# Optimization experiments

Measured on AMD Instinct MI355X. Metric: run time of the kernel, lower is better.

Reference implementation:

```python
import jax, jax.numpy as jnp
import numpy as np

B, C, CI, T, H, W = 4, 256, 128, 8, 28, 28
EPS = 1e-5


def setup_inputs() -> dict:
    key = jax.random.key(0)
    ks = jax.random.split(key, 12)
    s = 0.02
    return {
        "x": jax.random.normal(ks[0], (B, C, T, H, W), jnp.float32),
        "Wg": jax.random.normal(ks[1], (CI, C), jnp.float32) * s,
        "bg": jax.random.normal(ks[2], (CI,), jnp.float32) * s,
        "Wt": jax.random.normal(ks[3], (CI, C), jnp.float32) * s,
        "bt": jax.random.normal(ks[4], (CI,), jnp.float32) * s,
        "Wp": jax.random.normal(ks[5], (CI, C), jnp.float32) * s,
        "bp": jax.random.normal(ks[6], (CI,), jnp.float32) * s,
        "Ww": jax.random.normal(ks[7], (C, CI), jnp.float32) * s,
        "bw": jax.random.normal(ks[8], (C,), jnp.float32) * s,
        "gamma": jax.random.normal(ks[9], (C,), jnp.float32) * s + 1.0,
        "beta": jax.random.normal(ks[10], (C,), jnp.float32) * s,
        "rmean": jax.random.normal(ks[11], (C,), jnp.float32) * s,
        "rvar": jax.random.uniform(jax.random.fold_in(key, 99), (C,), jnp.float32, 0.5, 1.5),
    }


def reference(x, Wg, bg, Wt, bt, Wp, bp, Ww, bw, gamma, beta, rmean, rvar):
    b, c, t, h, w = x.shape
    n = t * h * w
    xf = x.reshape(b, c, n)                                   # [B,C,N]
    # 1x1x1 conv projections == per-position linear maps
    g = jnp.einsum('oc,bcn->bno', Wg, xf) + bg                # [B,N,Ci]
    th = jnp.einsum('oc,bcn->bno', Wt, xf) + bt               # [B,N,Ci]
    ph = jnp.einsum('oc,bcn->bon', Wp, xf) + bp[None, :, None]  # [B,Ci,N]
    f = jnp.einsum('bnc,bcm->bnm', th, ph)                    # [B,N,N] attention logits
    attn = jax.nn.softmax(f, axis=-1)
    y = jnp.einsum('bnm,bmo->bno', attn, g)                   # [B,N,Ci]
    wy = jnp.einsum('co,bno->bcn', Ww, y) + bw[None, :, None]  # [B,C,N]
    # BatchNorm3d (eval mode: running stats)
    inv = gamma / jnp.sqrt(rvar + EPS)
    wy = wy * inv[None, :, None] + (beta - rmean * inv)[None, :, None]
    z = wy + xf                                               # residual
    return z.reshape(b, c, t, h, w)
```

## Files before the change

kernel.cpp:

```cpp
#include <hip/hip_runtime.h>
#include <hip/hip_bf16.h>
#include <hip/hip_fp8.h>

#define BB 4
#define CC 256
#define CI 128
#define NN 6272
#define LOG2E 1.4426950408889634f

typedef __attribute__((ext_vector_type(8))) __bf16 bf16x8;
typedef __attribute__((ext_vector_type(4))) __bf16 bf16x4;
typedef __attribute__((ext_vector_type(4))) float f32x4;
typedef __attribute__((ext_vector_type(16))) float f32x16;

__device__ __forceinline__ void gll16(const void* g, void* l) {
  __builtin_amdgcn_global_load_lds(
      (const __attribute__((address_space(1))) void*)g,
      (__attribute__((address_space(3))) void*)l, 16, 0, 0);
}

__device__ __forceinline__ unsigned cvtpk_fp8(float a, float b) {
  unsigned r;
  asm("v_cvt_pk_fp8_f32 %0, %1, %2" : "=v"(r) : "v"(a), "v"(b));
  return r;
}

__device__ __forceinline__ unsigned char to_fp8(float v) {
  __hip_fp8_e4m3 t(v);
  return *reinterpret_cast<unsigned char*>(&t);
}

__global__ void nlb_prep(const float* __restrict__ Wg, const float* __restrict__ bg,
                         const float* __restrict__ Wt, const float* __restrict__ bt,
                         const float* __restrict__ Wp, const float* __restrict__ bp,
                         const float* __restrict__ Ww, const float* __restrict__ bw,
                         const float* __restrict__ gamma, const float* __restrict__ beta,
                         const float* __restrict__ rmean, const float* __restrict__ rvar,
                         __bf16* __restrict__ wall, float* __restrict__ ball,
                         __bf16* __restrict__ wwb, float* __restrict__ scale,
                         float* __restrict__ shift) {
  int idx = blockIdx.x * 256 + threadIdx.x;
  if (idx < 384 * 256) {
    int o = idx >> 8, c = idx & 255;
    float v, bv;
    if (o < 128)      { v = Wt[o * 256 + c] * LOG2E;  bv = bt[o] * LOG2E; }
    else if (o < 256) { v = Wp[(o - 128) * 256 + c]; bv = bp[o - 128]; }
    else              { v = Wg[(o - 256) * 256 + c]; bv = bg[o - 256]; }
    wall[idx] = (__bf16)v;
    if (c == 0) ball[o] = bv;
  } else if (idx < 384 * 256 + 256 * 128) {
    int i = idx - 384 * 256;
    wwb[i] = (__bf16)Ww[i];
  } else if (idx < 384 * 256 + 256 * 128 + 256) {
    int c = idx - (384 * 256 + 256 * 128);
    float inv = gamma[c] * rsqrtf(rvar[c] + 1e-5f);
    scale[c] = inv;
    shift[c] = (bw[c] - rmean[c]) * inv + beta[c];
  }
}

__launch_bounds__(256)
__global__ void nlb_proj(const float* __restrict__ x, const __bf16* __restrict__ wall,
                         const float* __restrict__ ball,
                         unsigned char* __restrict__ Q8, unsigned char* __restrict__ K8,
                         unsigned char* __restrict__ V8t) {
  const int nb = blockIdx.x;
  const int mb = blockIdx.y;
  const int b  = blockIdx.z;
  const int tid = threadIdx.x;
  const int lane = tid & 63, w = tid >> 6;
  const int n0 = nb * 64;
  const int m0 = mb * 64 + w * 16;
  const int r = lane & 15, g = lane >> 4;

  __shared__ __bf16 xl[64][40];

  const float* xb = x + (size_t)b * CC * NN;
  f32x4 acc[4] = {};

  const int snn = tid & 63;
  const int skg = tid >> 6;

  for (int k0 = 0; k0 < 256; k0 += 32) {
    bf16x8 tmp;
#pragma unroll
    for (int i = 0; i < 8; ++i)
      tmp[i] = (__bf16)xb[(size_t)(k0 + skg * 8 + i) * NN + n0 + snn];
    __syncthreads();
    *reinterpret_cast<bf16x8*>(&xl[snn][skg * 8]) = tmp;
    __syncthreads();

    bf16x8 afrag = *reinterpret_cast<const bf16x8*>(&wall[(size_t)(m0 + r) * 256 + k0 + g * 8]);
#pragma unroll
    for (int j = 0; j < 4; ++j) {
      bf16x8 bfrag = *reinterpret_cast<const bf16x8*>(&xl[j * 16 + r][g * 8]);
      acc[j] = __builtin_amdgcn_mfma_f32_16x16x32_bf16(afrag, bfrag, acc[j], 0, 0, 0);
    }
  }

  if (m0 < 256) {
    unsigned char* dst = (m0 < 128) ? Q8 : K8;
    const int obase = (m0 < 128) ? m0 : (m0 - 128);
#pragma unroll
    for (int j = 0; j < 4; ++j) {
      int n = n0 + j * 16 + r;
      union { unsigned char bch[4]; unsigned u; } pk;
#pragma unroll
      for (int reg = 0; reg < 4; ++reg) {
        int o = m0 + g * 4 + reg;
        pk.bch[reg] = to_fp8(acc[j][reg] + ball[o]);
      }
      *reinterpret_cast<unsigned*>(&dst[((size_t)b * NN + n) * CI + obase + g * 4]) = pk.u;
    }
  } else {
#pragma unroll
    for (int j = 0; j < 4; ++j) {
      int n = n0 + j * 16 + r;
#pragma unroll
      for (int reg = 0; reg < 4; ++reg) {
        int o = m0 + g * 4 + reg;
        float v = acc[j][reg] + ball[o];
        V8t[((size_t)b * CI + (o - 256)) * NN + n] = to_fp8(v);
      }
    }
  }
}

__launch_bounds__(256, 2)
__global__ void nlb_attn(const unsigned char* __restrict__ Q8,
                         const unsigned char* __restrict__ K8,
                         const unsigned char* __restrict__ V8t,
                         __bf16* __restrict__ Y) {
  const int bid = blockIdx.x;
  const int swz = (bid & 7) * 49 + (bid >> 3);
  const int b  = swz / 98;
  const int qb = swz % 98;
  const int tid = threadIdx.x, lane = tid & 63, w = tid >> 6;
  const int c = lane & 31, hi = lane >> 5;
  const int wq = w & 1, h = w >> 1;
  const int q0 = qb * 64 + wq * 32;

  const unsigned char* Qb = Q8  + (size_t)b * NN * CI;
  const char* Kc = (const char*)(K8 + (size_t)b * NN * CI);
  const char* Vc = (const char*)(V8t + (size_t)b * CI * NN);

  __shared__ __align__(16) char sm[32768];
  __shared__ float mls[2][2][64];

  const char* ks[2]; const char* vs[2];
#pragma unroll
  for (int i = 0; i < 2; ++i) {
    int p = i * 4096 + tid * 16;
    int kr = p >> 7, kcl = p & 127;
    ks[i] = Kc + (size_t)kr * 128 + (kcl ^ ((kr & 7) << 4));
    int vr = p >> 6, vcl = p & 63;
    vs[i] = Vc + (size_t)vr * NN + (vcl ^ ((vr & 3) << 4));
  }

  auto stage = [&](int bb, int t) {
    size_t ko = (size_t)t << 13;
    size_t vo = (size_t)t << 6;
    char* kl = sm + bb * 8192;
    char* vl = sm + 16384 + bb * 8192;
#pragma unroll
    for (int i = 0; i < 2; ++i) {
      gll16(ks[i] + ko, kl + i * 4096 + tid * 16);
      gll16(vs[i] + vo, vl + i * 4096 + tid * 16);
    }
  };

  long qf[8];
#pragma unroll
  for (int kc = 0; kc < 8; ++kc)
    qf[kc] = *reinterpret_cast<const long*>(&Qb[(size_t)(q0 + c) * CI + kc * 16 + hi * 8]);

  f32x16 yacc[4] = {};
  float m_r = -1e30f, l_r = 0.f;

  stage(0, 0);
  __syncthreads();

  const int kswz = (c & 7) << 4;
  const int vswz = (c & 3) << 4;

  int buf = 0;
  for (int t = 0; t < 98; ++t) {
    if (t + 1 < 98) stage(buf ^ 1, t + 1);
    const char* kl = sm + buf * 8192;
    const char* vl = sm + 16384 + buf * 8192;

    f32x16 s = {};
    __builtin_amdgcn_s_setprio(1);
#pragma unroll
    for (int kc = 0; kc < 8; ++kc) {
      long kf = *reinterpret_cast<const long*>(
          kl + (h * 32 + c) * 128 + ((kc * 16 + hi * 8) ^ kswz));
      s = __builtin_amdgcn_mfma_f32_32x32x16_fp8_fp8(kf, qf[kc], s, 0, 0, 0);
    }
    __builtin_amdgcn_s_setprio(0);

    float mx = fmaxf(fmaxf(fmaxf(s[0], s[1]), fmaxf(s[2], s[3])),
                     fmaxf(fmaxf(s[4], s[5]), fmaxf(s[6], s[7])));
    mx = fmaxf(mx, fmaxf(fmaxf(fmaxf(s[8], s[9]), fmaxf(s[10], s[11])),
                         fmaxf(fmaxf(s[12], s[13]), fmaxf(s[14], s[15]))));
    mx = fmaxf(mx, __shfl_xor(mx, 32));

    if (!__all(mx <= m_r + 2.f)) {
      float mnew = fmaxf(m_r, mx);
      float al = exp2f(m_r - mnew);
      m_r = mnew;
      l_r *= al;
      float alr[16];
#pragma unroll
      for (int reg = 0; reg < 16; ++reg)
        alr[reg] = __shfl(al, (reg & 3) + 8 * (reg >> 2) + 4 * hi);
#pragma unroll
      for (int cb = 0; cb < 4; ++cb)
#pragma unroll
        for (int reg = 0; reg < 16; ++reg)
          yacc[cb][reg] *= alr[reg];
    }

    float mb = m_r - 6.f;
    float ps = 0.f;
#pragma unroll
    for (int reg = 0; reg < 16; ++reg) {
      s[reg] = exp2f(s[reg] - mb);
      ps += s[reg];
    }
    ps += __shfl_xor(ps, 32);
    l_r += ps;

    unsigned pw[4];
#pragma unroll
    for (int i = 0; i < 4; ++i) {
      unsigned lo = cvtpk_fp8(s[4 * i + 0], s[4 * i + 1]);
      unsigned hi2 = cvtpk_fp8(s[4 * i + 2], s[4 * i + 3]);
      pw[i] = (hi2 << 16) | (lo & 0xffffu);
    }

    __builtin_amdgcn_s_setprio(1);
#pragma unroll
    for (int ch = 0; ch < 2; ++ch) {
      unsigned A = pw[ch * 2 + 0], B = pw[ch * 2 + 1];
      unsigned sX = (unsigned)__shfl_xor((int)(hi ? A : B), 32);
      unsigned plo = hi ? sX : A;
      unsigned phi = hi ? B : sX;
      long pa = (long)(((unsigned long long)phi << 32) | plo);
#pragma unroll
      for (int cb = 0; cb < 4; ++cb) {
        long vf = *reinterpret_cast<const long*>(
            vl + (cb * 32 + c) * 64 + ((h * 32 + ch * 16 + hi * 8) ^ vswz));
        yacc[cb] = __builtin_amdgcn_mfma_f32_32x32x16_fp8_fp8(pa, vf, yacc[cb], 0, 0, 0);
      }
    }
    __builtin_amdgcn_s_setprio(0);

    __syncthreads();
    buf ^= 1;
  }

  float* scr = (float*)sm;
  if (h == 1) {
    float* base = scr + wq * 4096;
#pragma unroll
    for (int cb = 0; cb < 4; ++cb)
#pragma unroll
      for (int reg = 0; reg < 16; ++reg)
        base[(cb * 16 + reg) * 64 + lane] = yacc[cb][reg];
    mls[wq][0][lane] = m_r;
    mls[wq][1][lane] = l_r;
  }
  __syncthreads();
  if (h == 0) {
    const float* base = scr + wq * 4096;
    float mB = mls[wq][0][lane], lB = mls[wq][1][lane];
    float mM = fmaxf(m_r, mB);
    float fA = exp2f(m_r - mM);
    float fB = exp2f(mB - mM);
    float il = 1.f / (l_r * fA + lB * fB);
    float faq[16], fbq[16], ilq[16];
#pragma unroll
    for (int reg = 0; reg < 16; ++reg) {
      int qloc = (reg & 3) + 8 * (reg >> 2) + 4 * hi;
      faq[reg] = __shfl(fA, qloc);
      fbq[reg] = __shfl(fB, qloc);
      ilq[reg] = __shfl(il, qloc);
    }
#pragma unroll
    for (int cb = 0; cb < 4; ++cb) {
#pragma unroll
      for (int reg = 0; reg < 16; ++reg) {
        int qloc = (reg & 3) + 8 * (reg >> 2) + 4 * hi;
        float v = (yacc[cb][reg] * faq[reg] + base[(cb * 16 + reg) * 64 + lane] * fbq[reg]) * ilq[reg];
        Y[((size_t)b * NN + q0 + qloc) * CI + cb * 32 + c] = (__bf16)v;
      }
    }
  }
}

__launch_bounds__(256)
__global__ void nlb_out(const __bf16* __restrict__ Y, const __bf16* __restrict__ wwb,
                        const float* __restrict__ scale, const float* __restrict__ shift,
                        const float* __restrict__ x, float* __restrict__ out) {
  const int nb = blockIdx.x;
  const int mb = blockIdx.y;
  const int b  = blockIdx.z;
  const int tid = threadIdx.x, lane = tid & 63, w = tid >> 6;
  const int r = lane & 15, g = lane >> 4;
  const int n0 = nb * 64, c0 = mb * 64 + w * 16;

  const __bf16* Yb = Y + (size_t)b * NN * CI;
  f32x4 acc[4] = {};
#pragma unroll
  for (int k0 = 0; k0 < 128; k0 += 32) {
    bf16x8 af = *reinterpret_cast<const bf16x8*>(&wwb[(size_t)(c0 + r) * CI + k0 + g * 8]);
#pragma unroll
    for (int j = 0; j < 4; ++j) {
      bf16x8 bfg = *reinterpret_cast<const bf16x8*>(
          &Yb[(size_t)(n0 + j * 16 + r) * CI + k0 + g * 8]);
      acc[j] = __builtin_amdgcn_mfma_f32_16x16x32_bf16(af, bfg, acc[j], 0, 0, 0);
    }
  }
  const float* xb = x + (size_t)b * CC * NN;
  float* ob = out + (size_t)b * CC * NN;
#pragma unroll
  for (int j = 0; j < 4; ++j) {
    int n = n0 + j * 16 + r;
#pragma unroll
    for (int reg = 0; reg < 4; ++reg) {
      int cc = c0 + g * 4 + reg;
      size_t off = (size_t)cc * NN + n;
      ob[off] = acc[j][reg] * scale[cc] + shift[cc] + xb[off];
    }
  }
}

extern "C" void kernel_launch(void* const* d_in, const int* in_sizes, int n_in,
                              void* d_out, int out_size, void* d_ws, size_t ws_size,
                              hipStream_t stream) {
  (void)in_sizes; (void)n_in; (void)out_size; (void)ws_size;
  const float* x     = (const float*)d_in[0];
  const float* Wg    = (const float*)d_in[1];
  const float* bg    = (const float*)d_in[2];
  const float* Wt    = (const float*)d_in[3];
  const float* bt    = (const float*)d_in[4];
  const float* Wp    = (const float*)d_in[5];
  const float* bp    = (const float*)d_in[6];
  const float* Ww    = (const float*)d_in[7];
  const float* bw    = (const float*)d_in[8];
  const float* gamma = (const float*)d_in[9];
  const float* beta  = (const float*)d_in[10];
  const float* rmean = (const float*)d_in[11];
  const float* rvar  = (const float*)d_in[12];
  float* out = (float*)d_out;

  char* ws = (char*)d_ws;
  __bf16* wall = (__bf16*)(ws + 0);
  float*  ball = (float*)(ws + 196608);
  __bf16* wwb  = (__bf16*)(ws + 198144);
  float*  scl  = (float*)(ws + 263680);
  float*  shf  = (float*)(ws + 264704);
  unsigned char* Q8 = (unsigned char*)(ws + 265728);
  unsigned char* K8 = (unsigned char*)(ws + 3476992);
  unsigned char* V8 = (unsigned char*)(ws + 6688256);
  __bf16* Yw   = (__bf16*)(ws + 9899520);

  nlb_prep<<<513, 256, 0, stream>>>(Wg, bg, Wt, bt, Wp, bp, Ww, bw, gamma, beta,
                                    rmean, rvar, wall, ball, wwb, scl, shf);
  nlb_proj<<<dim3(98, 6, 4), 256, 0, stream>>>(x, wall, ball, Q8, K8, V8);
  nlb_attn<<<392, 256, 0, stream>>>(Q8, K8, V8, Yw);
  nlb_out<<<dim3(98, 4, 4), 256, 0, stream>>>(Yw, wwb, scl, shf, x, out);
}
```

Before: 211.6 us.

## Replace direct global-to-LDS loads with register-staged copies into padded LDS tiles

Replaces the global_load_lds DMA staging of K and V tiles with ordinary global loads into registers, issued at the top of each iteration and written to LDS after the MFMA work. XOR swizzling is replaced by padded row strides (136 and 72 bytes) to avoid bank conflicts on the fragment reads. This aims to hide load latency behind compute, but it adds register pressure (16 extra dwords per thread under launch_bounds 256,2), more VALU/LDS write instructions, and a larger LDS footprint.

```diff
diff --git a/kernel.cpp b/kernel.cpp
--- a/kernel.cpp
+++ b/kernel.cpp
@@ -8,16 +8,15 @@
 #define NN 6272
 #define LOG2E 1.4426950408889634f
 
+#define KSTRIDE 136
+#define VSTRIDE 72
+#define KBUF (64 * KSTRIDE)
+#define VBUF (128 * VSTRIDE)
+
 typedef __attribute__((ext_vector_type(8))) __bf16 bf16x8;
 typedef __attribute__((ext_vector_type(4))) __bf16 bf16x4;
 typedef __attribute__((ext_vector_type(4))) float f32x4;
 typedef __attribute__((ext_vector_type(16))) float f32x16;
-
-__device__ __forceinline__ void gll16(const void* g, void* l) {
-  __builtin_amdgcn_global_load_lds(
-      (const __attribute__((address_space(1))) void*)g,
-      (__attribute__((address_space(3))) void*)l, 16, 0, 0);
-}
 
 __device__ __forceinline__ unsigned cvtpk_fp8(float a, float b) {
   unsigned r;
@@ -141,32 +140,35 @@
   const int q0 = qb * 64 + wq * 32;
 
   const unsigned char* Qb = Q8  + (size_t)b * NN * CI;
-  const char* Kc = (const char*)(K8 + (size_t)b * NN * CI);
-  const char* Vc = (const char*)(V8t + (size_t)b * CI * NN);
-
-  __shared__ __align__(16) char sm[32768];
+  const char* Kb = (const char*)(K8 + (size_t)b * NN * CI);
+  const char* Vb = (const char*)(V8t + (size_t)b * CI * NN);
+
+  __shared__ __align__(16) char sm[2 * KBUF + 2 * VBUF];
   __shared__ float mls[2][2][64];
 
-  const char* ks[2]; const char* vs[2];
-#pragma unroll
-  for (int i = 0; i < 2; ++i) {
-    int p = i * 4096 + tid * 16;
-    int kr = p >> 7, kcl = p & 127;
-    ks[i] = Kc + (size_t)kr * 128 + (kcl ^ ((kr & 7) << 4));
-    int vr = p >> 6, vcl = p & 63;
-    vs[i] = Vc + (size_t)vr * NN + (vcl ^ ((vr & 3) << 4));
-  }
-
-  auto stage = [&](int bb, int t) {
-    size_t ko = (size_t)t << 13;
-    size_t vo = (size_t)t << 6;
-    char* kl = sm + bb * 8192;
-    char* vl = sm + 16384 + bb * 8192;
-#pragma unroll
-    for (int i = 0; i < 2; ++i) {
-      gll16(ks[i] + ko, kl + i * 4096 + tid * 16);
-      gll16(vs[i] + vo, vl + i * 4096 + tid * 16);
-    }
+  uint4 gk0, gk1, gv0, gv1;
+  const char* vsrc_base = Vb + (size_t)(tid >> 1) * NN + (tid & 1) * 32;
+  auto gload = [&](int t) {
+    const char* ksrc = Kb + (size_t)t * 8192 + tid * 32;
+    const char* vsrc = vsrc_base + t * 64;
+    gk0 = *reinterpret_cast<const uint4*>(ksrc);
+    gk1 = *reinterpret_cast<const uint4*>(ksrc + 16);
+    gv0 = *reinterpret_cast<const uint4*>(vsrc);
+    gv1 = *reinterpret_cast<const uint4*>(vsrc + 16);
+  };
+  char* const kd_base = sm + (tid >> 2) * KSTRIDE + (tid & 3) * 32;
+  char* const vd_base = sm + 2 * KBUF + (tid >> 1) * VSTRIDE + (tid & 1) * 32;
+  auto swrite = [&](int bb) {
+    char* kd = kd_base + bb * KBUF;
+    *reinterpret_cast<uint2*>(kd + 0)  = make_uint2(gk0.x, gk0.y);
+    *reinterpret_cast<uint2*>(kd + 8)  = make_uint2(gk0.z, gk0.w);
+    *reinterpret_cast<uint2*>(kd + 16) = make_uint2(gk1.x, gk1.y);
+    *reinterpret_cast<uint2*>(kd + 24) = make_uint2(gk1.z, gk1.w);
+    char* vd = vd_base + bb * VBUF;
+    *reinterpret_cast<uint2*>(vd + 0)  = make_uint2(gv0.x, gv0.y);
+    *reinterpret_cast<uint2*>(vd + 8)  = make_uint2(gv0.z, gv0.w);
+    *reinterpret_cast<uint2*>(vd + 16) = make_uint2(gv1.x, gv1.y);
+    *reinterpret_cast<uint2*>(vd + 24) = make_uint2(gv1.z, gv1.w);
   };
 
   long qf[8];
@@ -177,24 +179,22 @@
   f32x16 yacc[4] = {};
   float m_r = -1e30f, l_r = 0.f;
 
-  stage(0, 0);
+  gload(0);
+  swrite(0);
   __syncthreads();
-
-  const int kswz = (c & 7) << 4;
-  const int vswz = (c & 3) << 4;
 
   int buf = 0;
   for (int t = 0; t < 98; ++t) {
-    if (t + 1 < 98) stage(buf ^ 1, t + 1);
-    const char* kl = sm + buf * 8192;
-    const char* vl = sm + 16384 + buf * 8192;
+    if (t + 1 < 98) gload(t + 1);
+    const char* kl = sm + buf * KBUF;
+    const char* vl = sm + 2 * KBUF + buf * VBUF;
 
     f32x16 s = {};
     __builtin_amdgcn_s_setprio(1);
 #pragma unroll
     for (int kc = 0; kc < 8; ++kc) {
       long kf = *reinterpret_cast<const long*>(
-          kl + (h * 32 + c) * 128 + ((kc * 16 + hi * 8) ^ kswz));
+          kl + (h * 32 + c) * KSTRIDE + kc * 16 + hi * 8);
       s = __builtin_amdgcn_mfma_f32_32x32x16_fp8_fp8(kf, qf[kc], s, 0, 0, 0);
     }
     __builtin_amdgcn_s_setprio(0);
@@ -250,12 +250,13 @@
 #pragma unroll
       for (int cb = 0; cb < 4; ++cb) {
         long vf = *reinterpret_cast<const long*>(
-            vl + (cb * 32 + c) * 64 + ((h * 32 + ch * 16 + hi * 8) ^ vswz));
+            vl + (cb * 32 + c) * VSTRIDE + h * 32 + ch * 16 + hi * 8);
         yacc[cb] = __builtin_amdgcn_mfma_f32_32x32x16_fp8_fp8(pa, vf, yacc[cb], 0, 0, 0);
       }
     }
     __builtin_amdgcn_s_setprio(0);
 
+    if (t + 1 < 98) swrite(buf ^ 1);
     __syncthreads();
     buf ^= 1;
   }
```

Measured after the change: 191.2 us. 1.11x faster.
